# Performance work log

Hardware: AMD Instinct MI355X
Metric: run time of the kernel (lower is better)

The kernel has to match this reference:

```python
import jax, jax.numpy as jnp
import numpy as np

E = 8      # num_expert
D = 1024   # d_model
H = 2048   # expert hidden (htoh4 size)
K = 2      # top_k
N = 2048   # tokens (batch*seq)


def setup_inputs() -> dict:
    key = jax.random.key(0)
    ks = jax.random.split(key, 4)
    sc = lambda k, shape, s: jax.random.normal(k, shape, jnp.float32) * s
    return {
        "inp": jax.random.normal(ks[0], (N, D), jnp.float32),
        "Wg": sc(ks[1], (D, E), D ** -0.5),          # NaiveGate linear
        "bg": jnp.zeros((E,), jnp.float32),
        "W1": sc(ks[2], (E, D, H), D ** -0.5),        # per-expert htoh4
        "b1": jnp.zeros((E, H), jnp.float32),
        "W2": sc(ks[3], (E, H, D), H ** -0.5),        # per-expert h4toh
        "b2": jnp.zeros((E, D), jnp.float32),
    }


def reference(inp, Wg, bg, W1, b1, W2, b2):
    # NaiveGate: linear -> top_k logits -> softmax over the k selected logits
    logits = inp @ Wg + bg                              # [N, E]
    top_val, top_idx = jax.lax.top_k(logits, K)         # [N, K]
    gate_score = jax.nn.softmax(top_val, axis=-1)       # [N, K]

    # Expert grouped compute. Reference computes every expert on every token
    # (exact math, no capacity dropping); combine selects the routed ones.
    h = jax.nn.gelu(jnp.einsum('nd,edh->neh', inp, W1) + b1)   # [N, E, H]
    y = jnp.einsum('neh,ehd->ned', h, W2) + b2                 # [N, E, D]

    # Combine: equivalent to bmm(gate_score[N,1,K], x[N,K,D]) after gather.
    comb = jnp.sum(jax.nn.one_hot(top_idx, E, dtype=inp.dtype)
                   * gate_score[..., None], axis=1)            # [N, E]
    return jnp.einsum('ne,ned->nd', comb, y)                   # [N, D]
```

## Files before the change

kernel.cpp:

```cpp
#include <hip/hip_runtime.h>
#include <math.h>

#define N_TOK 2048
#define DM    1024
#define HD    2048
#define NE    8
#define RMAX  5120
#define TMAX  40
#define KSPL  2

#define GATE_BLKS 512
#define XCVT_BLKS 1024
#define PREP_BLKS (GATE_BLKS + XCVT_BLKS)

typedef short short8 __attribute__((ext_vector_type(8)));
typedef unsigned short u16x8 __attribute__((ext_vector_type(8)));
typedef float f32x4  __attribute__((ext_vector_type(4)));

__device__ inline unsigned short f2b(float f) {
  unsigned int u = __float_as_uint(f);
  return (unsigned short)((u + 0x7FFFu + ((u >> 16) & 1u)) >> 16);
}
__device__ inline float b2f(unsigned short s) {
  return __uint_as_float(((unsigned int)s) << 16);
}
__device__ inline void gload_lds16(const void* g, void* l) {
  __builtin_amdgcn_global_load_lds(
      (const __attribute__((address_space(1))) unsigned int*)g,
      (__attribute__((address_space(3))) unsigned int*)l, 16, 0, 0);
}

__global__ __launch_bounds__(256) void prep_kernel(
    const float* __restrict__ inp, const float* __restrict__ Wg,
    const float* __restrict__ bg,
    int* __restrict__ top_idx, float* __restrict__ gate_w,
    unsigned short* __restrict__ Xb) {
  int bid = blockIdx.x;
  if (bid < GATE_BLKS) {
    int wave = threadIdx.x >> 6;
    int lane = threadIdx.x & 63;
    int n = bid * 4 + wave;
    float acc[NE];
#pragma unroll
    for (int e = 0; e < NE; ++e) acc[e] = 0.f;
    const float4* wg4 = reinterpret_cast<const float4*>(Wg);
#pragma unroll
    for (int i = 0; i < DM / 64; ++i) {
      int d = i * 64 + lane;
      float x = inp[n * DM + d];
      float4 w0 = wg4[d * 2 + 0];
      float4 w1 = wg4[d * 2 + 1];
      acc[0] += x * w0.x; acc[1] += x * w0.y; acc[2] += x * w0.z; acc[3] += x * w0.w;
      acc[4] += x * w1.x; acc[5] += x * w1.y; acc[6] += x * w1.z; acc[7] += x * w1.w;
    }
#pragma unroll
    for (int off = 32; off > 0; off >>= 1) {
#pragma unroll
      for (int e = 0; e < NE; ++e) acc[e] += __shfl_xor(acc[e], off);
    }
    if (lane == 0) {
      float v0 = -1e30f, v1 = -1e30f; int i0 = -1, i1 = -1;
#pragma unroll
      for (int e = 0; e < NE; ++e) {
        float v = acc[e] + bg[e];
        if (v > v0)      { v1 = v0; i1 = i0; v0 = v; i0 = e; }
        else if (v > v1) { v1 = v;  i1 = e; }
      }
      float e1 = expf(v1 - v0);
      float s  = 1.f + e1;
      top_idx[n * 2]     = i0;
      top_idx[n * 2 + 1] = i1;
      gate_w[n * 2]      = 1.f / s;
      gate_w[n * 2 + 1]  = e1 / s;
    }
  } else {
    int i = ((bid - GATE_BLKS) * 256 + threadIdx.x) * 8;
    float4 a = *(const float4*)(inp + i);
    float4 b = *(const float4*)(inp + i + 4);
    ushort4 pa, pb;
    pa.x = f2b(a.x); pa.y = f2b(a.y); pa.z = f2b(a.z); pa.w = f2b(a.w);
    pb.x = f2b(b.x); pb.y = f2b(b.y); pb.z = f2b(b.z); pb.w = f2b(b.w);
    *(ushort4*)(Xb + i)     = pa;
    *(ushort4*)(Xb + i + 4) = pb;
  }
}

__global__ __launch_bounds__(1024) void group_kernel(
    const int* __restrict__ top_idx,
    int* __restrict__ token_of, int* __restrict__ inv_g,
    int* __restrict__ tile_expert, int* __restrict__ tile_row0,
    int* __restrict__ n_tiles) {
  __shared__ int s_wtot[16];
  int tid = threadIdx.x, lane = tid & 63, wid = tid >> 6;
  int base = 0, tiles = 0;
  for (int e = 0; e < NE; ++e) {
    int cnt = 0;
#pragma unroll
    for (int c0 = 0; c0 < N_TOK; c0 += 1024) {
      int n = c0 + tid;
      int t0 = top_idx[n * 2], t1 = top_idx[n * 2 + 1];
      bool f = (t0 == e) || (t1 == e);
      int k = (t0 == e) ? 0 : 1;
      unsigned long long m = __ballot(f);
      int lp = __popcll(m & ((1ull << lane) - 1ull));
      if (lane == 0) s_wtot[wid] = __popcll(m);
      __syncthreads();
      int wbase = 0, tot = 0;
#pragma unroll
      for (int w = 0; w < 16; ++w) {
        int c = s_wtot[w];
        if (w < wid) wbase += c;
        tot += c;
      }
      if (f) {
        int pos = base + cnt + wbase + lp;
        token_of[pos] = n;
        inv_g[n * 2 + k] = pos;
      }
      cnt += tot;
      __syncthreads();
    }
    int padded = (cnt + 127) & ~127;
    for (int i = cnt + tid; i < padded; i += 1024) token_of[base + i] = -1;
    if (tid == 0) {
      for (int t = 0; t < padded / 128; ++t) {
        tile_expert[tiles + t] = e;
        tile_row0[tiles + t]   = base + t * 128;
      }
    }
    tiles += padded / 128;
    base  += padded;
    __syncthreads();
  }
  if (tid == 0) n_tiles[0] = tiles;
}

__global__ __launch_bounds__(256, 6) void ffn1_mfma(
    const unsigned short* __restrict__ Xb,
    const float* __restrict__ W1,
    const float* __restrict__ b1,
    const unsigned short* __restrict__ Xzero,
    const int* __restrict__ token_of, const int* __restrict__ tile_expert,
    const int* __restrict__ tile_row0, const int* __restrict__ n_tiles,
    unsigned short* __restrict__ Hbuf) {
  int lin  = blockIdx.x;
  int xcd  = lin & 7, slot = lin >> 3;
  int unit = xcd * 4 + slot / TMAX;
  int t    = slot % TMAX;
  if (t >= n_tiles[0]) return;
  int e    = tile_expert[t];
  int row0 = tile_row0[t];
  int h0   = unit * 64;
  __shared__ __align__(16) unsigned short Asl[2][128][32];
  __shared__ __align__(16) unsigned short Bsl[2][4][64][8];
  int tid = threadIdx.x, lane = tid & 63;
  int wid = tid >> 6, wr = wid >> 1, wc = wid & 1;
  int l15 = lane & 15, l4 = lane >> 4;
  int sw  = (l15 >> 1) & 3;

  int ar[2], asg[2], tk[2];
#pragma unroll
  for (int q = 0; q < 2; ++q) {
    int idx = tid + q * 256;
    ar[q]  = idx >> 2;
    asg[q] = (idx & 3) ^ ((ar[q] >> 1) & 3);
    tk[q]  = token_of[row0 + ar[q]];
  }
  int bcol = tid & 63, bks = tid >> 6;
  const float* W1e = W1 + (size_t)e * DM * HD;

  f32x4 acc[4][2] = {};
  float bvA[8], bvB[8];

  auto issueB = [&](int tt, float* bv) {
    const float* p = W1e + (size_t)(tt * 32 + bks * 8) * HD + h0 + bcol;
#pragma unroll
    for (int i = 0; i < 8; ++i) bv[i] = p[(size_t)i * HD];
  };
  auto packwrite = [&](const float* bv, int buf) {
    u16x8 o;
#pragma unroll
    for (int i = 0; i < 8; ++i) o[i] = f2b(bv[i]);
    *(u16x8*)&Bsl[buf][bks][bcol][0] = o;
  };
  auto issueA = [&](int tt, int buf) {
#pragma unroll
    for (int q = 0; q < 2; ++q) {
      int idx = tid + q * 256;
      const unsigned short* ga = (tk[q] < 0)
          ? Xzero
          : Xb + (size_t)tk[q] * DM + tt * 32 + asg[q] * 8;
      gload_lds16(ga, (char*)&Asl[buf][0][0] + (size_t)idx * 16);
    }
  };
  auto compute = [&](int buf) {
    short8 a[4], b[2];
#pragma unroll
    for (int m = 0; m < 4; ++m) {
      int R = wr * 64 + m * 16 + l15;
      a[m] = *(const short8*)((const char*)&Asl[buf][0][0] + R * 64 + ((l4 ^ sw) << 4));
    }
#pragma unroll
    for (int n = 0; n < 2; ++n)
      b[n] = *(const short8*)&Bsl[buf][l4][wc * 32 + n * 16 + l15][0];
#pragma unroll
    for (int m = 0; m < 4; ++m)
#pragma unroll
      for (int n = 0; n < 2; ++n)
        acc[m][n] = __builtin_amdgcn_mfma_f32_16x16x32_bf16(a[m], b[n], acc[m][n], 0, 0, 0);
  };

  issueB(0, bvA);
  issueA(0, 0);
  for (int kt = 0; kt < 32; kt += 2) {
    packwrite(bvA, 0);
    __syncthreads();
    if (kt + 1 < 32) { issueB(kt + 1, bvB); issueA(kt + 1, 1); }
    compute(0);
    packwrite(bvB, 1);
    __syncthreads();
    if (kt + 2 < 32) { issueB(kt + 2, bvA); issueA(kt + 2, 0); }
    compute(1);
  }

  float bias[2];
#pragma unroll
  for (int n = 0; n < 2; ++n) bias[n] = b1[e * HD + h0 + wc * 32 + n * 16 + l15];
#pragma unroll
  for (int m = 0; m < 4; ++m) {
#pragma unroll
    for (int n = 0; n < 2; ++n) {
      int col = h0 + wc * 32 + n * 16 + l15;
#pragma unroll
      for (int j = 0; j < 4; ++j) {
        int row = row0 + wr * 64 + m * 16 + l4 * 4 + j;
        float x = acc[m][n][j] + bias[n];
        float g = 0.5f * x * (1.f + tanhf(0.7978845608f * (x + 0.044715f * x * x * x)));
        Hbuf[(size_t)row * HD + col] = f2b(g);
      }
    }
  }
}

__global__ __launch_bounds__(256, 6) void ffn2_mfma(
    const unsigned short* __restrict__ Hbuf,
    const float* __restrict__ W2,
    const float* __restrict__ b2,
    const int* __restrict__ tile_expert, const int* __restrict__ tile_row0,
    const int* __restrict__ n_tiles,
    float* __restrict__ Ypart) {
  int lin  = blockIdx.x;
  int xcd  = lin & 7, slot = lin >> 3;
  int unit = xcd * 4 + slot / TMAX;
  int t    = slot % TMAX;
  if (t >= n_tiles[0]) return;
  int e    = tile_expert[t];
  int row0 = tile_row0[t];
  int d0   = (unit >> 1) * 64;
  int ks   = unit & 1;
  int kbase = ks * (HD / KSPL);
  __shared__ __align__(16) unsigned short Asl[2][128][32];
  __shared__ __align__(16) unsigned short Bsl[2][4][64][8];
  int tid = threadIdx.x, lane = tid & 63;
  int wid = tid >> 6, wr = wid >> 1, wc = wid & 1;
  int l15 = lane & 15, l4 = lane >> 4;
  int sw  = (l15 >> 1) & 3;

  int ar[2], asg[2];
#pragma unroll
  for (int q = 0; q < 2; ++q) {
    int idx = tid + q * 256;
    ar[q]  = idx >> 2;
    asg[q] = (idx & 3) ^ ((ar[q] >> 1) & 3);
  }
  int bcol = tid & 63, bks = tid >> 6;
  const float* W2e = W2 + (size_t)e * HD * DM + (size_t)kbase * DM;

  f32x4 acc[4][2] = {};
  float bvA[8], bvB[8];

  auto issueB = [&](int tt, float* bv) {
    const float* p = W2e + (size_t)(tt * 32 + bks * 8) * DM + d0 + bcol;
#pragma unroll
    for (int i = 0; i < 8; ++i) bv[i] = p[(size_t)i * DM];
  };
  auto packwrite = [&](const float* bv, int buf) {
    u16x8 o;
#pragma unroll
    for (int i = 0; i < 8; ++i) o[i] = f2b(bv[i]);
    *(u16x8*)&Bsl[buf][bks][bcol][0] = o;
  };
  auto issueA = [&](int tt, int buf) {
#pragma unroll
    for (int q = 0; q < 2; ++q) {
      int idx = tid + q * 256;
      const unsigned short* ga =
          Hbuf + (size_t)(row0 + ar[q]) * HD + kbase + tt * 32 + asg[q] * 8;
      gload_lds16(ga, (char*)&Asl[buf][0][0] + (size_t)idx * 16);
    }
  };
  auto compute = [&](int buf) {
    short8 a[4], b[2];
#pragma unroll
    for (int m = 0; m < 4; ++m) {
      int R = wr * 64 + m * 16 + l15;
      a[m] = *(const short8*)((const char*)&Asl[buf][0][0] + R * 64 + ((l4 ^ sw) << 4));
    }
#pragma unroll
    for (int n = 0; n < 2; ++n)
      b[n] = *(const short8*)&Bsl[buf][l4][wc * 32 + n * 16 + l15][0];
#pragma unroll
    for (int m = 0; m < 4; ++m)
#pragma unroll
      for (int n = 0; n < 2; ++n)
        acc[m][n] = __builtin_amdgcn_mfma_f32_16x16x32_bf16(a[m], b[n], acc[m][n], 0, 0, 0);
  };

  const int NT = HD / KSPL / 32;
  issueB(0, bvA);
  issueA(0, 0);
  for (int kt = 0; kt < NT; kt += 2) {
    packwrite(bvA, 0);
    __syncthreads();
    if (kt + 1 < NT) { issueB(kt + 1, bvB); issueA(kt + 1, 1); }
    compute(0);
    packwrite(bvB, 1);
    __syncthreads();
    if (kt + 2 < NT) { issueB(kt + 2, bvA); issueA(kt + 2, 0); }
    compute(1);
  }

  float bias[2];
#pragma unroll
  for (int n = 0; n < 2; ++n)
    bias[n] = (ks == 0) ? b2[e * DM + d0 + wc * 32 + n * 16 + l15] : 0.f;
  float* Yp = Ypart + (size_t)ks * RMAX * DM;
#pragma unroll
  for (int m = 0; m < 4; ++m) {
#pragma unroll
    for (int n = 0; n < 2; ++n) {
      int col = d0 + wc * 32 + n * 16 + l15;
#pragma unroll
      for (int j = 0; j < 4; ++j) {
        int row = row0 + wr * 64 + m * 16 + l4 * 4 + j;
        Yp[(size_t)row * DM + col] = acc[m][n][j] + bias[n];
      }
    }
  }
}

__global__ void combine_kernel(const float* __restrict__ Ypart,
                               const int* __restrict__ inv_g,
                               const float* __restrict__ gate_w,
                               float* __restrict__ out) {
  int n = blockIdx.x;
  int r0 = inv_g[n * 2], r1 = inv_g[n * 2 + 1];
  float g0 = gate_w[n * 2], g1 = gate_w[n * 2 + 1];
  int i = threadIdx.x;
  const float4* y00 = (const float4*)(Ypart + (size_t)r0 * DM);
  const float4* y01 = (const float4*)(Ypart + (size_t)(RMAX + r0) * DM);
  const float4* y10 = (const float4*)(Ypart + (size_t)r1 * DM);
  const float4* y11 = (const float4*)(Ypart + (size_t)(RMAX + r1) * DM);
  float4 a0 = y00[i], a1 = y01[i], b0 = y10[i], b1 = y11[i];
  float4 rv;
  rv.x = g0 * (a0.x + a1.x) + g1 * (b0.x + b1.x);
  rv.y = g0 * (a0.y + a1.y) + g1 * (b0.y + b1.y);
  rv.z = g0 * (a0.z + a1.z) + g1 * (b0.z + b1.z);
  rv.w = g0 * (a0.w + a1.w) + g1 * (b0.w + b1.w);
  *(float4*)(out + (size_t)n * DM + i * 4) = rv;
}

extern "C" void kernel_launch(void* const* d_in, const int* in_sizes, int n_in,
                              void* d_out, int out_size, void* d_ws, size_t ws_size,
                              hipStream_t stream) {
  const float* inp = (const float*)d_in[0];
  const float* Wg  = (const float*)d_in[1];
  const float* bg  = (const float*)d_in[2];
  const float* W1  = (const float*)d_in[3];
  const float* b1  = (const float*)d_in[4];
  const float* W2  = (const float*)d_in[5];
  const float* b2  = (const float*)d_in[6];
  float* out = (float*)d_out;

  char* ws = (char*)d_ws;
  size_t off = 0;
  auto alloc = [&](size_t bytes) {
    size_t o = off;
    off = (off + bytes + 255) & ~(size_t)255;
    return o;
  };
  int*   top_idx     = (int*)  (ws + alloc(N_TOK * 2 * sizeof(int)));
  float* gate_w      = (float*)(ws + alloc(N_TOK * 2 * sizeof(float)));
  int*   token_of    = (int*)  (ws + alloc(RMAX * sizeof(int)));
  int*   inv_g       = (int*)  (ws + alloc(N_TOK * 2 * sizeof(int)));
  int*   tile_expert = (int*)  (ws + alloc(TMAX * sizeof(int)));
  int*   tile_row0   = (int*)  (ws + alloc(TMAX * sizeof(int)));
  int*   n_tiles     = (int*)  (ws + alloc(sizeof(int)));
  unsigned short* Xzero = (unsigned short*)(ws + alloc(DM * 2));
  unsigned short* Xb    = (unsigned short*)(ws + alloc((size_t)N_TOK * DM * 2));
  unsigned short* Hbuf  = (unsigned short*)(ws + alloc((size_t)RMAX * HD * 2));
  float*          Ypart = (float*)(ws + alloc((size_t)KSPL * RMAX * DM * 4));
  (void)ws_size;

  hipMemsetAsync(Xzero, 0, DM * 2, stream);
  prep_kernel<<<PREP_BLKS, 256, 0, stream>>>(inp, Wg, bg, top_idx, gate_w, Xb);
  group_kernel<<<1, 1024, 0, stream>>>(top_idx, token_of, inv_g,
                                       tile_expert, tile_row0, n_tiles);
  ffn1_mfma<<<8 * 4 * TMAX, 256, 0, stream>>>(
      Xb, W1, b1, Xzero, token_of, tile_expert, tile_row0, n_tiles, Hbuf);
  ffn2_mfma<<<8 * 4 * TMAX, 256, 0, stream>>>(
      Hbuf, W2, b2, tile_expert, tile_row0, n_tiles, Ypart);
  combine_kernel<<<N_TOK, 256, 0, stream>>>(Ypart, inv_g, gate_w, out);
}
```

Measured before the change: 146.1 us.

## Pre-convert W2 to packed bf16 layout and load B tiles directly to LDS

Adds prep blocks that convert W2 to bf16 in a k-packed-by-8 layout each call, and changes ffn2 to fetch B tiles with asynchronous global-to-LDS loads instead of strided fp32 register loads plus conversion. This halves the bytes ffn2 reads for W2 across tiles and removes register staging. The cost is an extra full pass over W2 in the prep kernel and a 32MB workspace buffer.

```diff
diff --git a/kernel.cpp b/kernel.cpp
--- a/kernel.cpp
+++ b/kernel.cpp
@@ -11,7 +11,8 @@
 
 #define GATE_BLKS 512
 #define XCVT_BLKS 1024
-#define PREP_BLKS (GATE_BLKS + XCVT_BLKS)
+#define WCV2_BLKS 2048
+#define PREP_BLKS (GATE_BLKS + XCVT_BLKS + WCV2_BLKS)
 
 typedef short short8 __attribute__((ext_vector_type(8)));
 typedef unsigned short u16x8 __attribute__((ext_vector_type(8)));
@@ -32,9 +33,9 @@
 
 __global__ __launch_bounds__(256) void prep_kernel(
     const float* __restrict__ inp, const float* __restrict__ Wg,
-    const float* __restrict__ bg,
+    const float* __restrict__ bg,  const float* __restrict__ W2,
     int* __restrict__ top_idx, float* __restrict__ gate_w,
-    unsigned short* __restrict__ Xb) {
+    unsigned short* __restrict__ Xb, unsigned short* __restrict__ W2C) {
   int bid = blockIdx.x;
   if (bid < GATE_BLKS) {
     int wave = threadIdx.x >> 6;
@@ -73,7 +74,7 @@
       gate_w[n * 2]      = 1.f / s;
       gate_w[n * 2 + 1]  = e1 / s;
     }
-  } else {
+  } else if (bid < GATE_BLKS + XCVT_BLKS) {
     int i = ((bid - GATE_BLKS) * 256 + threadIdx.x) * 8;
     float4 a = *(const float4*)(inp + i);
     float4 b = *(const float4*)(inp + i + 4);
@@ -82,6 +83,27 @@
     pb.x = f2b(b.x); pb.y = f2b(b.y); pb.z = f2b(b.z); pb.w = f2b(b.w);
     *(ushort4*)(Xb + i)     = pa;
     *(ushort4*)(Xb + i + 4) = pb;
+  } else {
+    int wb = bid - (GATE_BLKS + XCVT_BLKS);
+    int z  = wb >> 8;
+    int r  = wb & 255;
+    int gx = r & 3, gy = r >> 2;
+    const float* src = W2 + (size_t)z * HD * DM;
+    unsigned short* dst = W2C + (size_t)z * HD * DM;
+    int n0 = gx * 256, k0 = gy * 32;
+    int t  = threadIdx.x;
+    int cg = t & 63, kg = t >> 6;
+    const float* s = src + (size_t)(k0 + kg * 8) * DM + n0 + cg * 4;
+    float4 v[8];
+#pragma unroll
+    for (int i = 0; i < 8; ++i) v[i] = *(const float4*)(s + (size_t)i * DM);
+#pragma unroll
+    for (int c = 0; c < 4; ++c) {
+      u16x8 o;
+      o[0] = f2b(v[0][c]); o[1] = f2b(v[1][c]); o[2] = f2b(v[2][c]); o[3] = f2b(v[3][c]);
+      o[4] = f2b(v[4][c]); o[5] = f2b(v[5][c]); o[6] = f2b(v[6][c]); o[7] = f2b(v[7][c]);
+      *(u16x8*)(dst + ((size_t)(k0 / 8 + kg) * DM + n0 + cg * 4 + c) * 8) = o;
+    }
   }
 }
 
@@ -244,7 +266,7 @@
 
 __global__ __launch_bounds__(256, 6) void ffn2_mfma(
     const unsigned short* __restrict__ Hbuf,
-    const float* __restrict__ W2,
+    const unsigned short* __restrict__ W2C,
     const float* __restrict__ b2,
     const int* __restrict__ tile_expert, const int* __restrict__ tile_row0,
     const int* __restrict__ n_tiles,
@@ -259,6 +281,7 @@
   int d0   = (unit >> 1) * 64;
   int ks   = unit & 1;
   int kbase = ks * (HD / KSPL);
+  int kb0   = kbase >> 3;
   __shared__ __align__(16) unsigned short Asl[2][128][32];
   __shared__ __align__(16) unsigned short Bsl[2][4][64][8];
   int tid = threadIdx.x, lane = tid & 63;
@@ -274,23 +297,11 @@
     asg[q] = (idx & 3) ^ ((ar[q] >> 1) & 3);
   }
   int bcol = tid & 63, bks = tid >> 6;
-  const float* W2e = W2 + (size_t)e * HD * DM + (size_t)kbase * DM;
+  const unsigned short* W2e = W2C + (size_t)e * HD * DM;
 
   f32x4 acc[4][2] = {};
-  float bvA[8], bvB[8];
-
-  auto issueB = [&](int tt, float* bv) {
-    const float* p = W2e + (size_t)(tt * 32 + bks * 8) * DM + d0 + bcol;
-#pragma unroll
-    for (int i = 0; i < 8; ++i) bv[i] = p[(size_t)i * DM];
-  };
-  auto packwrite = [&](const float* bv, int buf) {
-    u16x8 o;
-#pragma unroll
-    for (int i = 0; i < 8; ++i) o[i] = f2b(bv[i]);
-    *(u16x8*)&Bsl[buf][bks][bcol][0] = o;
-  };
-  auto issueA = [&](int tt, int buf) {
+
+  auto issueAB = [&](int tt, int buf) {
 #pragma unroll
     for (int q = 0; q < 2; ++q) {
       int idx = tid + q * 256;
@@ -298,6 +309,9 @@
           Hbuf + (size_t)(row0 + ar[q]) * HD + kbase + tt * 32 + asg[q] * 8;
       gload_lds16(ga, (char*)&Asl[buf][0][0] + (size_t)idx * 16);
     }
+    const unsigned short* gb =
+        W2e + ((size_t)(kb0 + tt * 4 + bks) * DM + d0 + bcol) * 8;
+    gload_lds16(gb, (char*)&Bsl[buf][0][0] + (size_t)tid * 16);
   };
   auto compute = [&](int buf) {
     short8 a[4], b[2];
@@ -317,16 +331,13 @@
   };
 
   const int NT = HD / KSPL / 32;
-  issueB(0, bvA);
-  issueA(0, 0);
+  issueAB(0, 0);
   for (int kt = 0; kt < NT; kt += 2) {
-    packwrite(bvA, 0);
     __syncthreads();
-    if (kt + 1 < NT) { issueB(kt + 1, bvB); issueA(kt + 1, 1); }
+    if (kt + 1 < NT) issueAB(kt + 1, 1);
     compute(0);
-    packwrite(bvB, 1);
     __syncthreads();
-    if (kt + 2 < NT) { issueB(kt + 2, bvA); issueA(kt + 2, 0); }
+    if (kt + 2 < NT) issueAB(kt + 2, 0);
     compute(1);
   }
 
@@ -398,17 +409,19 @@
   int*   n_tiles     = (int*)  (ws + alloc(sizeof(int)));
   unsigned short* Xzero = (unsigned short*)(ws + alloc(DM * 2));
   unsigned short* Xb    = (unsigned short*)(ws + alloc((size_t)N_TOK * DM * 2));
+  unsigned short* W2C   = (unsigned short*)(ws + alloc((size_t)NE * HD * DM * 2));
   unsigned short* Hbuf  = (unsigned short*)(ws + alloc((size_t)RMAX * HD * 2));
   float*          Ypart = (float*)(ws + alloc((size_t)KSPL * RMAX * DM * 4));
   (void)ws_size;
 
   hipMemsetAsync(Xzero, 0, DM * 2, stream);
-  prep_kernel<<<PREP_BLKS, 256, 0, stream>>>(inp, Wg, bg, top_idx, gate_w, Xb);
+  prep_kernel<<<PREP_BLKS, 256, 0, stream>>>(inp, Wg, bg, W2,
+                                             top_idx, gate_w, Xb, W2C);
   group_kernel<<<1, 1024, 0, stream>>>(top_idx, token_of, inv_g,
                                        tile_expert, tile_row0, n_tiles);
   ffn1_mfma<<<8 * 4 * TMAX, 256, 0, stream>>>(
       Xb, W1, b1, Xzero, token_of, tile_expert, tile_row0, n_tiles, Hbuf);
   ffn2_mfma<<<8 * 4 * TMAX, 256, 0, stream>>>(
-      Hbuf, W2, b2, tile_expert, tile_row0, n_tiles, Ypart);
+      Hbuf, W2C, b2, tile_expert, tile_row0, n_tiles, Ypart);
   combine_kernel<<<N_TOK, 256, 0, stream>>>(Ypart, inv_g, gate_w, out);
 }
```

After: 149.4 us. +2.2%, slower.

## Deepen FFN GEMM pipelines to triple-buffered LDS with manual waitcnt barriers

Applied to the files above, without the earlier changes.

Both expert GEMM kernels move from a double-buffered LDS loop to a three-stage ring, prefetching two K-tiles ahead. The __syncthreads is replaced by explicit s_waitcnt vmcnt/lgkmcnt and a raw s_barrier so outstanding global loads can stay in flight across iterations. The aim is to hide more global-load latency behind MFMA compute. In exchange, shared memory per block rises by half and launch bounds drop from 6 to 4 blocks per CU, lowering occupancy. The hand-picked vmcnt(10) count depends on how many loads each issue call emits, so it could be wrong.

```diff
diff --git a/kernel.cpp b/kernel.cpp
--- a/kernel.cpp
+++ b/kernel.cpp
@@ -135,7 +135,7 @@
   if (tid == 0) n_tiles[0] = tiles;
 }
 
-__global__ __launch_bounds__(256, 6) void ffn1_mfma(
+__global__ __launch_bounds__(256, 4) void ffn1_mfma(
     const unsigned short* __restrict__ Xb,
     const float* __restrict__ W1,
     const float* __restrict__ b1,
@@ -151,8 +151,8 @@
   int e    = tile_expert[t];
   int row0 = tile_row0[t];
   int h0   = unit * 64;
-  __shared__ __align__(16) unsigned short Asl[2][128][32];
-  __shared__ __align__(16) unsigned short Bsl[2][4][64][8];
+  __shared__ __align__(16) unsigned short Asl[3][128][32];
+  __shared__ __align__(16) unsigned short Bsl[3][4][64][8];
   int tid = threadIdx.x, lane = tid & 63;
   int wid = tid >> 6, wr = wid >> 1, wc = wid & 1;
   int l15 = lane & 15, l4 = lane >> 4;
@@ -210,17 +210,23 @@
         acc[m][n] = __builtin_amdgcn_mfma_f32_16x16x32_bf16(a[m], b[n], acc[m][n], 0, 0, 0);
   };
 
-  issueB(0, bvA);
-  issueA(0, 0);
-  for (int kt = 0; kt < 32; kt += 2) {
-    packwrite(bvA, 0);
-    __syncthreads();
-    if (kt + 1 < 32) { issueB(kt + 1, bvB); issueA(kt + 1, 1); }
-    compute(0);
-    packwrite(bvB, 1);
-    __syncthreads();
-    if (kt + 2 < 32) { issueB(kt + 2, bvA); issueA(kt + 2, 0); }
-    compute(1);
+  issueB(0, bvA); issueA(0, 0);
+  issueB(1, bvB); issueA(1, 1);
+  int buf = 0;
+  for (int kt = 0; kt < 32; ++kt) {
+    packwrite((kt & 1) ? bvB : bvA, buf);
+    if (kt < 31) asm volatile("s_waitcnt vmcnt(10)" ::: "memory");
+    else         asm volatile("s_waitcnt vmcnt(0)"  ::: "memory");
+    asm volatile("s_waitcnt lgkmcnt(0)" ::: "memory");
+    __builtin_amdgcn_s_barrier();
+    __builtin_amdgcn_sched_barrier(0);
+    compute(buf);
+    if (kt + 2 < 32) {
+      int nb = buf + 2; if (nb >= 3) nb -= 3;
+      issueB(kt + 2, (kt & 1) ? bvB : bvA);
+      issueA(kt + 2, nb);
+    }
+    if (++buf == 3) buf = 0;
   }
 
   float bias[2];
@@ -242,7 +248,7 @@
   }
 }
 
-__global__ __launch_bounds__(256, 6) void ffn2_mfma(
+__global__ __launch_bounds__(256, 4) void ffn2_mfma(
     const unsigned short* __restrict__ Hbuf,
     const float* __restrict__ W2,
     const float* __restrict__ b2,
@@ -259,8 +265,8 @@
   int d0   = (unit >> 1) * 64;
   int ks   = unit & 1;
   int kbase = ks * (HD / KSPL);
-  __shared__ __align__(16) unsigned short Asl[2][128][32];
-  __shared__ __align__(16) unsigned short Bsl[2][4][64][8];
+  __shared__ __align__(16) unsigned short Asl[3][128][32];
+  __shared__ __align__(16) unsigned short Bsl[3][4][64][8];
   int tid = threadIdx.x, lane = tid & 63;
   int wid = tid >> 6, wr = wid >> 1, wc = wid & 1;
   int l15 = lane & 15, l4 = lane >> 4;
@@ -317,17 +323,23 @@
   };
 
   const int NT = HD / KSPL / 32;
-  issueB(0, bvA);
-  issueA(0, 0);
-  for (int kt = 0; kt < NT; kt += 2) {
-    packwrite(bvA, 0);
-    __syncthreads();
-    if (kt + 1 < NT) { issueB(kt + 1, bvB); issueA(kt + 1, 1); }
-    compute(0);
-    packwrite(bvB, 1);
-    __syncthreads();
-    if (kt + 2 < NT) { issueB(kt + 2, bvA); issueA(kt + 2, 0); }
-    compute(1);
+  issueB(0, bvA); issueA(0, 0);
+  issueB(1, bvB); issueA(1, 1);
+  int buf = 0;
+  for (int kt = 0; kt < NT; ++kt) {
+    packwrite((kt & 1) ? bvB : bvA, buf);
+    if (kt < NT - 1) asm volatile("s_waitcnt vmcnt(10)" ::: "memory");
+    else             asm volatile("s_waitcnt vmcnt(0)"  ::: "memory");
+    asm volatile("s_waitcnt lgkmcnt(0)" ::: "memory");
+    __builtin_amdgcn_s_barrier();
+    __builtin_amdgcn_sched_barrier(0);
+    compute(buf);
+    if (kt + 2 < NT) {
+      int nb = buf + 2; if (nb >= 3) nb -= 3;
+      issueB(kt + 2, (kt & 1) ? bvB : bvA);
+      issueA(kt + 2, nb);
+    }
+    if (++buf == 3) buf = 0;
   }
 
   float bias[2];
```

Result: slower. 168.0 us (+14.9%).
